# Kernel tuning notes

Measured on AMD Instinct MI355X. Metric: run time of the kernel, lower is better.

The kernel has to match this reference:

```python
import jax, jax.numpy as jnp
import numpy as np

B, S, D, H = 4, 2048, 1024, 16
HD = D // H  # 64


def setup_inputs() -> dict:
    key = jax.random.key(0)
    ks = jax.random.split(key, 8)
    s = 0.02
    return {
        "inp_values": jax.random.normal(ks[0], (B, S, D), jnp.float32),
        "inp_keys": jax.random.normal(ks[1], (B, S, D), jnp.float32),
        "inp_queries": jax.random.normal(ks[2], (B, S, D), jnp.float32),
        # per-head projection weights, torch nn.Linear(head_dims, head_dims, bias=False): y = x @ W.T
        "Wv": jax.random.normal(ks[3], (HD, HD), jnp.float32) * s,
        "Wk": jax.random.normal(ks[4], (HD, HD), jnp.float32) * s,
        "Wq": jax.random.normal(ks[5], (HD, HD), jnp.float32) * s,
        # output projection nn.Linear(D, D) with bias
        "Wo": jax.random.normal(ks[6], (D, D), jnp.float32) * s,
        "bo": jax.random.normal(ks[7], (D,), jnp.float32) * s,
    }


def reference(inp_values, inp_keys, inp_queries, Wv, Wk, Wq, Wo, bo):
    b, sq, _ = inp_queries.shape
    sk = inp_values.shape[1]
    v = inp_values.reshape(b, sk, H, HD)
    k = inp_keys.reshape(b, sk, H, HD)
    q = inp_queries.reshape(b, sq, H, HD)
    # per-head linear: x @ W.T
    v = jnp.einsum('bshd,ed->bshe', v, Wv)
    k = jnp.einsum('bshd,ed->bshe', k, Wk)
    q = jnp.einsum('bshd,ed->bshe', q, Wq)
    # scores scaled by 1/sqrt(input_dims) as in the original (not head_dims)
    scores = jnp.einsum('bqhd,bkhd->bhqk', q, k) / jnp.sqrt(jnp.float32(D))
    attn = jax.nn.softmax(scores, axis=-1)  # [B,H,Q,K]
    out = jnp.einsum('bhqk,bkhd->bqhd', attn, v).reshape(b, sq, D)
    return out @ Wo.T + bo
```

## Files before the change

kernel.cpp:

```cpp
#include <hip/hip_runtime.h>
#include <hip/hip_bf16.h>

#define B_ 4
#define S_ 2048
#define D_ 1024
#define H_ 16
#define HD_ 64

typedef __attribute__((ext_vector_type(8))) short bf16x8;
typedef __attribute__((ext_vector_type(4))) short bf16x4;
typedef __attribute__((ext_vector_type(4))) float f32x4;

#define MFMA32(a, b, c) __builtin_amdgcn_mfma_f32_16x16x32_bf16(a, b, c, 0, 0, 0)

#define KSWZ(r) ((((r) & 3)) ^ ((((r) >> 3) & 1) << 2))

__device__ __forceinline__ float fast_exp2(float x) {
#if __has_builtin(__builtin_amdgcn_exp2f)
  return __builtin_amdgcn_exp2f(x);
#else
  return exp2f(x);
#endif
}

__device__ __forceinline__ float fast_rcp(float x) {
#if __has_builtin(__builtin_amdgcn_rcpf)
  return __builtin_amdgcn_rcpf(x);
#else
  return 1.0f / x;
#endif
}

__device__ __forceinline__ short f2bf(float x) {
  union { float f; unsigned u; } v; v.f = x;
  unsigned r = (v.u + 0x7fffu + ((v.u >> 16) & 1u)) >> 16;
  return (short)(r & 0xffffu);
}

__device__ __forceinline__ unsigned pack_hi16(float a, float b) {
  union { float f; unsigned u; } ua, ub; ua.f = a; ub.f = b;
  return __builtin_amdgcn_perm(ub.u, ua.u, 0x07060302u);
}

__device__ __forceinline__ void gl_lds16(const short* g, void* l) {
  __builtin_amdgcn_global_load_lds(
      (const __attribute__((address_space(1))) unsigned*)(const void*)g,
      (__attribute__((address_space(3))) unsigned*)l, 16, 0, 0);
}

__global__ __launch_bounds__(256) void qkv_proj2(
    const float* __restrict__ inpV, const float* __restrict__ inpK,
    const float* __restrict__ inpQ, const float* __restrict__ Wv,
    const float* __restrict__ Wk, const float* __restrict__ Wq,
    const float* __restrict__ Wo, short* __restrict__ wob,
    short* __restrict__ vt, short* __restrict__ kp, short* __restrict__ qp) {
  __shared__ bf16x8 xbuf[1024];
  __shared__ bf16x8 wbuf[512];
  int bid = blockIdx.x;
  int t = bid >> 10;
  int tid = threadIdx.x, wave = tid >> 6, lane = tid & 63;
  int quad = lane >> 4, l15 = lane & 15;

  if (t == 3) {
    int i = (bid & 511) * 256 + tid;
    const float4* src = (const float4*)Wo + i * 2;
    float4 a = src[0], b = src[1];
    bf16x8 o;
    o[0] = f2bf(a.x); o[1] = f2bf(a.y); o[2] = f2bf(a.z); o[3] = f2bf(a.w);
    o[4] = f2bf(b.x); o[5] = f2bf(b.y); o[6] = f2bf(b.z); o[7] = f2bf(b.w);
    ((bf16x8*)wob)[i] = o;
    return;
  }

  int bh = (bid >> 4) & 63;
  int st = bid & 15;
  int b = bh >> 4, h = bh & 15;
  int s0 = st * 128;
  const float* inp = (t == 0) ? inpV : (t == 1) ? inpK : inpQ;
  const float* W = (t == 0) ? Wv : (t == 1) ? Wk : Wq;
  float wscale = (t == 2) ? (0.03125f * 1.4426950408889634f) : 1.0f;

#pragma unroll
  for (int u = 0; u < 2; ++u) {
    int slot = tid + u * 256;
    int row = slot >> 3, g = slot & 7;
    const float4* wp = (const float4*)(W + row * 64 + g * 8);
    float4 w0 = wp[0], w1 = wp[1];
    bf16x8 o;
    o[0] = f2bf(w0.x * wscale); o[1] = f2bf(w0.y * wscale);
    o[2] = f2bf(w0.z * wscale); o[3] = f2bf(w0.w * wscale);
    o[4] = f2bf(w1.x * wscale); o[5] = f2bf(w1.y * wscale);
    o[6] = f2bf(w1.z * wscale); o[7] = f2bf(w1.w * wscale);
    wbuf[row * 8 + (g ^ (row & 7))] = o;
  }
  const float* xg = inp + (b * S_ + s0) * D_ + h * HD_;
#pragma unroll
  for (int u = 0; u < 4; ++u) {
    int slot = tid + u * 256;
    int row = slot >> 3, g = slot & 7;
    const float4* xp = (const float4*)(xg + row * D_ + g * 8);
    float4 x0 = xp[0], x1 = xp[1];
    bf16x8 o;
    o[0] = f2bf(x0.x); o[1] = f2bf(x0.y); o[2] = f2bf(x0.z); o[3] = f2bf(x0.w);
    o[4] = f2bf(x1.x); o[5] = f2bf(x1.y); o[6] = f2bf(x1.z); o[7] = f2bf(x1.w);
    xbuf[row * 8 + (g ^ (row & 7))] = o;
  }
  __syncthreads();

  if (t == 0) {
    f32x4 acc[2][4];
#pragma unroll
    for (int mt = 0; mt < 2; mt++)
#pragma unroll
      for (int nt = 0; nt < 4; nt++) { acc[mt][nt][0]=0.f; acc[mt][nt][1]=0.f; acc[mt][nt][2]=0.f; acc[mt][nt][3]=0.f; }
#pragma unroll
    for (int ks = 0; ks < 2; ++ks) {
      bf16x8 af[2], bfr[4];
#pragma unroll
      for (int mt = 0; mt < 2; ++mt) {
        int row = wave * 32 + mt * 16 + l15;
        af[mt] = xbuf[row * 8 + ((ks * 4 + quad) ^ (row & 7))];
      }
#pragma unroll
      for (int nt = 0; nt < 4; ++nt) {
        int row = nt * 16 + l15;
        bfr[nt] = wbuf[row * 8 + ((ks * 4 + quad) ^ (row & 7))];
      }
#pragma unroll
      for (int mt = 0; mt < 2; ++mt)
#pragma unroll
        for (int nt = 0; nt < 4; ++nt)
          acc[mt][nt] = MFMA32(af[mt], bfr[nt], acc[mt][nt]);
    }
    short* vb = vt + bh * 64 * S_;
#pragma unroll
    for (int mt = 0; mt < 2; ++mt)
#pragma unroll
      for (int nt = 0; nt < 4; ++nt) {
        bf16x4 pk;
#pragma unroll
        for (int r = 0; r < 4; ++r) pk[r] = f2bf(acc[mt][nt][r]);
        int e = nt * 16 + l15;
        int s = s0 + wave * 32 + mt * 16 + quad * 4;
        *(bf16x4*)(vb + e * S_ + s) = pk;
      }
  } else {
    f32x4 acc[4][2];
#pragma unroll
    for (int mt = 0; mt < 4; mt++)
#pragma unroll
      for (int nt = 0; nt < 2; nt++) { acc[mt][nt][0]=0.f; acc[mt][nt][1]=0.f; acc[mt][nt][2]=0.f; acc[mt][nt][3]=0.f; }
#pragma unroll
    for (int ks = 0; ks < 2; ++ks) {
      bf16x8 af[4], bfr[2];
#pragma unroll
      for (int mt = 0; mt < 4; ++mt) {
        int row = mt * 16 + l15;
        af[mt] = wbuf[row * 8 + ((ks * 4 + quad) ^ (row & 7))];
      }
#pragma unroll
      for (int nt = 0; nt < 2; ++nt) {
        int row = wave * 32 + nt * 16 + l15;
        bfr[nt] = xbuf[row * 8 + ((ks * 4 + quad) ^ (row & 7))];
      }
#pragma unroll
      for (int mt = 0; mt < 4; ++mt)
#pragma unroll
        for (int nt = 0; nt < 2; ++nt)
          acc[mt][nt] = MFMA32(af[mt], bfr[nt], acc[mt][nt]);
    }
    short* ob = ((t == 1) ? kp : qp) + bh * S_ * 64;
#pragma unroll
    for (int mt = 0; mt < 4; ++mt)
#pragma unroll
      for (int nt = 0; nt < 2; ++nt) {
        bf16x4 pk;
#pragma unroll
        for (int r = 0; r < 4; ++r) pk[r] = f2bf(acc[mt][nt][r]);
        int s = s0 + wave * 32 + nt * 16 + l15;
        int e = mt * 16 + quad * 4;
        *(bf16x4*)(ob + s * 64 + e) = pk;
      }
  }
}

__global__ __launch_bounds__(64, 2) void attention(
    const short* __restrict__ qp, const short* __restrict__ kp,
    const short* __restrict__ vt, short* __restrict__ ao) {
  __shared__ bf16x8 kbuf[2][256];
  __shared__ bf16x8 vbuf[2][256];
  int bid = blockIdx.x;
  int qt = bid >> 6;
  int bh = bid & 63;
  int lane = threadIdx.x & 63;
  int quad = lane >> 4, l15 = lane & 15;

  const short* qb = qp + (bh * S_ + qt * 64 + l15) * 64;
  bf16x8 bq[4][2];
#pragma unroll
  for (int qg = 0; qg < 4; ++qg) {
    bq[qg][0] = *(const bf16x8*)(qb + qg * 1024 + quad * 8);
    bq[qg][1] = *(const bf16x8*)(qb + qg * 1024 + 32 + quad * 8);
  }

  const f32x4 fzero = {0.f, 0.f, 0.f, 0.f};
  f32x4 o[4][4];
#pragma unroll
  for (int qg = 0; qg < 4; qg++)
#pragma unroll
    for (int dt = 0; dt < 4; dt++) o[qg][dt] = fzero;
  f32x4 lacc[4];
#pragma unroll
  for (int qg = 0; qg < 4; qg++) lacc[qg] = fzero;

  short one_bf = (short)0x3F80;
  bf16x8 ones8;
#pragma unroll
  for (int j = 0; j < 8; ++j) ones8[j] = (l15 == 0) ? one_bf : (short)0;

  const short* kg = kp + bh * S_ * 64;
  const short* vg = vt + bh * 64 * S_;

  const short* ksrc[4];
  const short* vsrc[4];
#pragma unroll
  for (int u = 0; u < 4; ++u) {
    int slot = lane + u * 64;
    int kr = slot >> 3, kgg = (slot & 7) ^ KSWZ(kr);
    ksrc[u] = kg + kr * 64 + kgg * 8;
    int vr = slot >> 2, vgg = (slot & 3) ^ (vr & 3);
    vsrc[u] = vg + vr * S_ + vgg * 8;
  }

#pragma unroll
  for (int u = 0; u < 4; ++u) gl_lds16(ksrc[u], &kbuf[0][u * 64]);
#pragma unroll
  for (int u = 0; u < 4; ++u) gl_lds16(vsrc[u], &vbuf[0][u * 64]);

  int krp0 = ((l15 >> 2) << 3) + (l15 & 3);

  int aslot0[2], aslot1[2], vslot[4];
#pragma unroll
  for (int nt = 0; nt < 2; ++nt) {
    int krow = krp0 + nt * 4;
    aslot0[nt] = krow * 8 + ((0 + quad) ^ KSWZ(krow));
    aslot1[nt] = krow * 8 + ((4 + quad) ^ KSWZ(krow));
  }
#pragma unroll
  for (int dt = 0; dt < 4; ++dt) {
    int d = dt * 16 + l15;
    vslot[dt] = d * 4 + (quad ^ (d & 3));
  }

#define ATTN_BODY(P, T)                                                     \
  do {                                                                      \
    int ktn = ((T) + 1) & 63; \
    _Pragma("unroll")                                                       \
    for (int u = 0; u < 4; ++u)                                             \
      gl_lds16(ksrc[u] + ktn * 2048, &kbuf[(P) ^ 1][u * 64]);               \
    _Pragma("unroll")                                                       \
    for (int u = 0; u < 4; ++u)                                             \
      gl_lds16(vsrc[u] + ktn * 32, &vbuf[(P) ^ 1][u * 64]);                 \
    asm volatile("s_waitcnt vmcnt(8)" ::: "memory");     \
    __builtin_amdgcn_sched_barrier(0);                                      \
    union Frag { unsigned u[4]; bf16x8 v; } pa[4];                          \
    _Pragma("unroll")                                                       \
    for (int nt = 0; nt < 2; ++nt) {                                        \
      bf16x8 ak0 = kbuf[(P)][aslot0[nt]];                                   \
      bf16x8 ak1 = kbuf[(P)][aslot1[nt]];                                   \
      _Pragma("unroll")                                                     \
      for (int qg = 0; qg < 4; ++qg) {                                      \
        f32x4 c = MFMA32(ak0, bq[qg][0], fzero);                            \
        c = MFMA32(ak1, bq[qg][1], c);                                      \
        float e0 = fast_exp2(c[0]), e1 = fast_exp2(c[1]);                   \
        float e2 = fast_exp2(c[2]), e3 = fast_exp2(c[3]);                   \
        pa[qg].u[nt * 2 + 0] = pack_hi16(e0, e1);                           \
        pa[qg].u[nt * 2 + 1] = pack_hi16(e2, e3);                           \
      }                                                                     \
    }                                                                       \
    __builtin_amdgcn_s_setprio(1);                                          \
    _Pragma("unroll")                                                       \
    for (int qg = 0; qg < 4; ++qg)                                          \
      lacc[qg] = MFMA32(pa[qg].v, ones8, lacc[qg]);                         \
    _Pragma("unroll")                                                       \
    for (int dt = 0; dt < 4; ++dt) {                                        \
      bf16x8 bv = vbuf[(P)][vslot[dt]];                                     \
      _Pragma("unroll")                                                     \
      for (int qg = 0; qg < 4; ++qg)                                        \
        o[qg][dt] = MFMA32(pa[qg].v, bv, o[qg][dt]);                        \
    }                                                                       \
    __builtin_amdgcn_s_setprio(0);                                          \
  } while (0)

  for (int kt = 0; kt < 64; kt += 2) {
    ATTN_BODY(0, kt);
    ATTN_BODY(1, kt + 1);
  }
#undef ATTN_BODY

  asm volatile("s_waitcnt vmcnt(0)" ::: "memory");

  int b = bh >> 4, h = bh & 15;
#pragma unroll
  for (int qg = 0; qg < 4; ++qg) {
    float inv[4];
#pragma unroll
    for (int r = 0; r < 4; ++r) {
      float ls = __shfl(lacc[qg][r], lane & 48, 64);
      inv[r] = fast_rcp(ls);
    }
#pragma unroll
    for (int dt = 0; dt < 4; ++dt)
#pragma unroll
      for (int r = 0; r < 4; ++r) {
        int srow = qt * 64 + qg * 16 + quad * 4 + r;
        ao[(b * S_ + srow) * D_ + h * 64 + dt * 16 + l15] =
            f2bf(o[qg][dt][r] * inv[r]);
      }
  }
}

__global__ __launch_bounds__(256) void outproj(const short* __restrict__ A,
                                               const short* __restrict__ Bw,
                                               const float* __restrict__ bo,
                                               float* __restrict__ out) {
  __shared__ bf16x8 sa[2][1024];
  __shared__ bf16x8 sb[2][1024];
  int bid = blockIdx.x;
  int m0 = (bid >> 3) * 128, n0 = (bid & 7) * 128;
  int tid = threadIdx.x, wave = tid >> 6, lane = tid & 63;
  int quad = lane >> 4, l15 = lane & 15;
  int wm = (wave >> 1) * 64, wn = (wave & 1) * 64;
  f32x4 acc[4][4];
#pragma unroll
  for (int mt = 0; mt < 4; mt++)
#pragma unroll
    for (int nt = 0; nt < 4; nt++) { acc[mt][nt][0]=0.f; acc[mt][nt][1]=0.f; acc[mt][nt][2]=0.f; acc[mt][nt][3]=0.f; }

  const short* asrc[4];
  const short* bsrc[4];
#pragma unroll
  for (int u = 0; u < 4; ++u) {
    int slot = tid + u * 256;
    int row = slot >> 3, g = (slot & 7) ^ (row & 7);
    asrc[u] = A + (m0 + row) * 1024 + g * 8;
    bsrc[u] = Bw + (n0 + row) * 1024 + g * 8;
  }
#pragma unroll
  for (int u = 0; u < 4; ++u) {
    gl_lds16(asrc[u], &sa[0][tid + u * 256]);
    gl_lds16(bsrc[u], &sb[0][tid + u * 256]);
  }

  int p = 0;
  for (int k0 = 0; k0 < 1024; k0 += 64) {
    __syncthreads();
    int kn = (k0 + 64) & 1023;
#pragma unroll
    for (int u = 0; u < 4; ++u) {
      gl_lds16(asrc[u] + kn, &sa[p ^ 1][tid + u * 256]);
      gl_lds16(bsrc[u] + kn, &sb[p ^ 1][tid + u * 256]);
    }
#pragma unroll
    for (int ks = 0; ks < 2; ++ks) {
      bf16x8 af[4], bf[4];
#pragma unroll
      for (int mt = 0; mt < 4; ++mt) {
        int row = wm + mt * 16 + l15;
        af[mt] = sa[p][row * 8 + ((ks * 4 + quad) ^ (row & 7))];
      }
#pragma unroll
      for (int nt = 0; nt < 4; ++nt) {
        int row = wn + nt * 16 + l15;
        bf[nt] = sb[p][row * 8 + ((ks * 4 + quad) ^ (row & 7))];
      }
#pragma unroll
      for (int mt = 0; mt < 4; ++mt)
#pragma unroll
        for (int nt = 0; nt < 4; ++nt)
          acc[mt][nt] = MFMA32(af[mt], bf[nt], acc[mt][nt]);
    }
    p ^= 1;
  }
#pragma unroll
  for (int nt = 0; nt < 4; ++nt) {
    int n = n0 + wn + nt * 16 + l15;
    float bov = bo[n];
#pragma unroll
    for (int mt = 0; mt < 4; ++mt)
#pragma unroll
      for (int r = 0; r < 4; r++) {
        int m = m0 + wm + mt * 16 + quad * 4 + r;
        out[m * 1024 + n] = acc[mt][nt][r] + bov;
      }
  }
}

extern "C" void kernel_launch(void* const* d_in, const int* in_sizes, int n_in,
                              void* d_out, int out_size, void* d_ws,
                              size_t ws_size, hipStream_t stream) {
  const float* inpV = (const float*)d_in[0];
  const float* inpK = (const float*)d_in[1];
  const float* inpQ = (const float*)d_in[2];
  const float* Wv = (const float*)d_in[3];
  const float* Wk = (const float*)d_in[4];
  const float* Wq = (const float*)d_in[5];
  const float* Wo = (const float*)d_in[6];
  const float* bo = (const float*)d_in[7];
  float* out = (float*)d_out;

  char* ws = (char*)d_ws;
  short* vt = (short*)(ws);
  short* kp = (short*)(ws + (16u << 20));
  short* qp = (short*)(ws + (32u << 20));
  short* ao = (short*)(ws + (48u << 20));
  short* wob = (short*)(ws + (64u << 20));

  qkv_proj2<<<dim3(3584), dim3(256), 0, stream>>>(inpV, inpK, inpQ, Wv, Wk, Wq,
                                                  Wo, wob, vt, kp, qp);
  attention<<<dim3(2048), dim3(64), 0, stream>>>(qp, kp, vt, ao);
  outproj<<<dim3(512), dim3(256), 0, stream>>>(ao, wob, bo, out);
}
```

Measured before the change: 259.3 us.

## Software-pipeline attention loop so PV MFMAs of previous tile overlap current exp

```diff
diff --git a/kernel.cpp b/kernel.cpp
--- a/kernel.cpp
+++ b/kernel.cpp
@@ -252,7 +252,26 @@
     vslot[dt] = d * 4 + (quad ^ (d & 3));
   }
 
-#define ATTN_BODY(P, T)                                                     \
+  union Frag { unsigned u[4]; bf16x8 v; };
+  Frag paA[4], paB[4];
+  bf16x8 bvA[4], bvB[4];
+
+#define PV_BLOCK(PA, BV)                                                    \
+  do {                                                                      \
+    __builtin_amdgcn_s_setprio(1);                                          \
+    _Pragma("unroll")                                                       \
+    for (int qg = 0; qg < 4; ++qg)                                          \
+      lacc[qg] = MFMA32(PA[qg].v, ones8, lacc[qg]);                         \
+    _Pragma("unroll")                                                       \
+    for (int dt = 0; dt < 4; ++dt) {                                        \
+      _Pragma("unroll")                                                     \
+      for (int qg = 0; qg < 4; ++qg)                                        \
+        o[qg][dt] = MFMA32(PA[qg].v, BV[dt], o[qg][dt]);                    \
+    }                                                                       \
+    __builtin_amdgcn_s_setprio(0);                                          \
+  } while (0)
+
+#define BODY(P, T, PA_CUR, BV_CUR, PA_PREV, BV_PREV, DO_PV)                 \
   do {                                                                      \
     int ktn = ((T) + 1) & 63; \
     _Pragma("unroll")                                                       \
@@ -263,40 +282,41 @@
       gl_lds16(vsrc[u] + ktn * 32, &vbuf[(P) ^ 1][u * 64]);                 \
     asm volatile("s_waitcnt vmcnt(8)" ::: "memory");     \
     __builtin_amdgcn_sched_barrier(0);                                      \
-    union Frag { unsigned u[4]; bf16x8 v; } pa[4];                          \
+    f32x4 c[2][4];                                                          \
     _Pragma("unroll")                                                       \
     for (int nt = 0; nt < 2; ++nt) {                                        \
       bf16x8 ak0 = kbuf[(P)][aslot0[nt]];                                   \
       bf16x8 ak1 = kbuf[(P)][aslot1[nt]];                                   \
       _Pragma("unroll")                                                     \
       for (int qg = 0; qg < 4; ++qg) {                                      \
-        f32x4 c = MFMA32(ak0, bq[qg][0], fzero);                            \
-        c = MFMA32(ak1, bq[qg][1], c);                                      \
-        float e0 = fast_exp2(c[0]), e1 = fast_exp2(c[1]);                   \
-        float e2 = fast_exp2(c[2]), e3 = fast_exp2(c[3]);                   \
-        pa[qg].u[nt * 2 + 0] = pack_hi16(e0, e1);                           \
-        pa[qg].u[nt * 2 + 1] = pack_hi16(e2, e3);                           \
+        c[nt][qg] = MFMA32(ak0, bq[qg][0], fzero);                          \
+        c[nt][qg] = MFMA32(ak1, bq[qg][1], c[nt][qg]);                      \
       }                                                                     \
     }                                                                       \
-    __builtin_amdgcn_s_setprio(1);                                          \
-    _Pragma("unroll")                                                       \
-    for (int qg = 0; qg < 4; ++qg)                                          \
-      lacc[qg] = MFMA32(pa[qg].v, ones8, lacc[qg]);                         \
-    _Pragma("unroll")                                                       \
-    for (int dt = 0; dt < 4; ++dt) {                                        \
-      bf16x8 bv = vbuf[(P)][vslot[dt]];                                     \
+    _Pragma("unroll")                                                       \
+    for (int dt = 0; dt < 4; ++dt) BV_CUR[dt] = vbuf[(P)][vslot[dt]];       \
+    if (DO_PV) PV_BLOCK(PA_PREV, BV_PREV); \
+    _Pragma("unroll")                                                       \
+    for (int nt = 0; nt < 2; ++nt) {                                        \
       _Pragma("unroll")                                                     \
-      for (int qg = 0; qg < 4; ++qg)                                        \
-        o[qg][dt] = MFMA32(pa[qg].v, bv, o[qg][dt]);                        \
+      for (int qg = 0; qg < 4; ++qg) {                                      \
+        float e0 = fast_exp2(c[nt][qg][0]), e1 = fast_exp2(c[nt][qg][1]);   \
+        float e2 = fast_exp2(c[nt][qg][2]), e3 = fast_exp2(c[nt][qg][3]);   \
+        PA_CUR[qg].u[nt * 2 + 0] = pack_hi16(e0, e1);                       \
+        PA_CUR[qg].u[nt * 2 + 1] = pack_hi16(e2, e3);                       \
+      }                                                                     \
     }                                                                       \
-    __builtin_amdgcn_s_setprio(0);                                          \
   } while (0)
 
-  for (int kt = 0; kt < 64; kt += 2) {
-    ATTN_BODY(0, kt);
-    ATTN_BODY(1, kt + 1);
-  }
-#undef ATTN_BODY
+  BODY(0, 0, paA, bvA, paB, bvB, 0);
+  for (int kt = 1; kt < 63; kt += 2) {
+    BODY(1, kt, paB, bvB, paA, bvA, 1);
+    BODY(0, kt + 1, paA, bvA, paB, bvB, 1);
+  }
+  BODY(1, 63, paB, bvB, paA, bvA, 1);
+  PV_BLOCK(paB, bvB);
+#undef BODY
+#undef PV_BLOCK
 
   asm volatile("s_waitcnt vmcnt(0)" ::: "memory");
 
```

Result: no change. 260.7 us (+0.6%).
